# Performance work log

Hardware: AMD Instinct MI355X
Metric: run time of the kernel (lower is better)

## Reference

```python
import jax, jax.numpy as jnp
import numpy as np

K = 1024
D = 256
BETA = 0.25


def setup_inputs() -> dict:
    key = jax.random.key(0)
    k1, k2 = jax.random.split(key)
    latents = jax.random.normal(k1, (32, D, 32, 32), dtype=jnp.float32)
    # nn.Embedding init: uniform(-1/K, 1/K)
    embedding = jax.random.uniform(k2, (K, D), dtype=jnp.float32,
                                   minval=-1.0 / K, maxval=1.0 / K)
    return {"latents": latents, "embedding": embedding}


def reference(latents, embedding):
    # latents: [B, D, H, W] -> [B, H, W, D]
    x = jnp.transpose(latents, (0, 2, 3, 1))
    input_shape = x.shape
    flat = x.reshape(-1, D)  # [N, D]

    # squared-L2 distances to codebook: [N, K]
    distances = (jnp.sum(flat ** 2, axis=1, keepdims=True)
                 + jnp.sum(embedding ** 2, axis=1)
                 - 2.0 * flat @ embedding.T)
    encoding_indices = jnp.argmin(distances, axis=1)  # [N]

    # one-hot encodings (returned output); quantize via direct gather
    encodings = jax.nn.one_hot(encoding_indices, K, dtype=latents.dtype)  # [N, K]
    quantized = embedding[encoding_indices].reshape(input_shape)  # [B, H, W, D]

    e_latent_loss = jnp.mean((jax.lax.stop_gradient(quantized) - x) ** 2)
    q_latent_loss = jnp.mean((quantized - jax.lax.stop_gradient(x)) ** 2)
    loss = q_latent_loss + BETA * e_latent_loss

    # straight-through estimator
    quantized_st = x + jax.lax.stop_gradient(quantized - x)

    avg_probs = jnp.mean(encodings, axis=0)  # [K]
    perplexity = jnp.exp(-jnp.sum(avg_probs * jnp.log(avg_probs + 1e-10)))

    return (loss,
            jnp.transpose(quantized_st, (0, 3, 1, 2)),  # [B, D, H, W]
            perplexity,
            encodings)
```

## Files before the change

kernel.cpp:

```cpp
#include <hip/hip_runtime.h>
#include <stdint.h>
#include <math.h>

typedef float  f32x4 __attribute__((ext_vector_type(4)));
typedef float  f32x2 __attribute__((ext_vector_type(2)));
typedef short  s16x8 __attribute__((ext_vector_type(8)));
typedef short  s16x4 __attribute__((ext_vector_type(4)));

#define KC   1024
#define DD   256
#define NR   32768

#define WS_HIST   0
#define WS_ACC    4096
#define WS_E2     8192
#define WS_IDX    12288
#define WS_PANEL  143360
#define WS_PART   671744

#define ENC_OFF   8388610ULL

#define A_OFF   0
#define B_OFF   32768
#define E2_OFF  65536
#define SMEM_SZ 67584

#define GLD16(gp, lp) __builtin_amdgcn_global_load_lds(                      \
    (const __attribute__((address_space(1))) uint32_t*)(gp),                 \
    (__attribute__((address_space(3))) uint32_t*)(lp), 16, 0, 0)

#define WAITVM(N) asm volatile("s_waitcnt vmcnt(" #N ")" ::: "memory")
#define PHASEBAR() do { __builtin_amdgcn_s_barrier();                        \
                        __builtin_amdgcn_sched_barrier(0); } while (0)

__device__ __forceinline__ short f2bf(float f) {
    uint32_t u = __builtin_bit_cast(uint32_t, f);
    uint32_t r = (u + 0x7FFFu + ((u >> 16) & 1u)) >> 16;
    return (short)r;
}

__global__ void k_prep(const float* __restrict__ emb, char* __restrict__ ws) {
    int tid = threadIdx.x;
    if (blockIdx.x == 0) {
        uint32_t* hist = (uint32_t*)(ws + WS_HIST);
        #pragma unroll
        for (int j = 0; j < 4; j++) hist[tid * 4 + j] = 0u;
        if (tid < 2) ((float*)(ws + WS_ACC))[tid] = 0.f;
    }
    int wid = tid >> 6, lane = tid & 63;
    int code = blockIdx.x * 4 + wid;
    const float* row = emb + (size_t)code * DD;
    f32x4 v = *(const f32x4*)(row + lane * 4);
    s16x4 b;
    b[0] = f2bf(v.x); b[1] = f2bf(v.y); b[2] = f2bf(v.z); b[3] = f2bf(v.w);
    *(s16x4*)((short*)(ws + WS_PANEL) + (size_t)code * DD + lane * 4) = b;
    float ss = v.x * v.x + v.y * v.y + v.z * v.z + v.w * v.w;
    #pragma unroll
    for (int off = 1; off < 64; off <<= 1) ss += __shfl_xor(ss, off);
    if (lane == 0) ((float*)(ws + WS_E2))[code] = ss;
}

__global__ __launch_bounds__(256, 2) void k_argmin(const float* __restrict__ latents,
                                                   char* __restrict__ ws) {
    const char*  panelb = (const char*)(ws + WS_PANEL);
    const float* e2g    = (const float*)(ws + WS_E2);
    float*       acc    = (float*)(ws + WS_ACC);

    __shared__ __align__(16) char smem[SMEM_SZ];

    int t     = threadIdx.x;
    int lane  = t & 63;
    int wid   = t >> 6;
    int g     = lane >> 4, r16 = lane & 15;
    int rowgrp = blockIdx.x >> 1;
    int chalf  = blockIdx.x & 1;
    int nbase  = rowgrp * 128;
    int b      = nbase >> 10;
    int hwbase = nbase & 1023;
    const char* pbase = panelb + (size_t)chalf * 262144;

    if (t < 128) {
        f32x4 ev = *(const f32x4*)(e2g + chalf * 512 + t * 4);
        *(f32x4*)(smem + E2_OFF + t * 16) = ev;
    }

    float xs = 0.f;
    s16x8 af[2][8];
    int rg = (t & 15) * 4;
    int dp = (t >> 4) * 2;
    int wb = 4 * ((t >> 4) & 3);

    #pragma unroll
    for (int h = 0; h < 2; h++) {
        const float* base = latents + (size_t)b * 262144 + hwbase + h * 64 + rg;
        #pragma unroll
        for (int i = 0; i < 8; i++) {
            int d = dp + i * 32;
            f32x4 v0 = *(const f32x4*)(base + (size_t)d * 1024);
            f32x4 v1 = *(const f32x4*)(base + (size_t)(d + 1) * 1024);
            xs += v0.x*v0.x + v0.y*v0.y + v0.z*v0.z + v0.w*v0.w;
            xs += v1.x*v1.x + v1.y*v1.y + v1.z*v1.z + v1.w*v1.w;
            int qb = d >> 3;
            #pragma unroll
            for (int q = 0; q < 4; q++) {
                int slot = rg + q;
                uint32_t pk = (uint32_t)(uint16_t)f2bf(v0[q])
                            | ((uint32_t)(uint16_t)f2bf(v1[q]) << 16);
                int quad = qb ^ (slot & 7);
                *(uint32_t*)(smem + A_OFF + slot * 512 + quad * 16 + wb) = pk;
            }
        }
        __syncthreads();
        if ((wid >> 1) == h) {
            int slotbase = (wid & 1) * 32;
            #pragma unroll
            for (int rt = 0; rt < 2; rt++) {
                #pragma unroll
                for (int kt = 0; kt < 8; kt++) {
                    int slot = slotbase + rt * 16 + r16;
                    int quad = (kt * 4 + g) ^ (slot & 7);
                    af[rt][kt] = *(const s16x8*)(smem + A_OFF + slot * 512 + quad * 16);
                }
            }
        }
        __syncthreads();
    }
    if (chalf == 0) {
        #pragma unroll
        for (int off = 1; off < 64; off <<= 1) xs += __shfl_xor(xs, off);
        if (lane == 0) atomicAdd(acc + 0, xs);
    }

    float vmin[2][4];
    int   vidx[2][4];
    #pragma unroll
    for (int rt = 0; rt < 2; rt++)
        #pragma unroll
        for (int j = 0; j < 4; j++) { vmin[rt][j] = 3.4e38f; vidx[rt][j] = 0; }

    const float* E2l = (const float*)(smem + E2_OFF);
    int codeglob = chalf * 512;

    auto stage = [&](int c) {
        const char* srcc = pbase + (size_t)c * 8192;
        char* dstb = smem + B_OFF + (size_t)(c & 3) * 8192;
        #pragma unroll
        for (int i = 0; i < 2; i++) {
            uint32_t off = i * 4096 + wid * 1024;
            uint32_t so  = off + lane * 16;
            uint32_t ssw = so ^ (((so >> 9) & 7u) << 4);
            GLD16(srcc + ssw, dstb + off);
        }
    };
    auto compute = [&](int c) {
        int cbase = c * 16;
        float e2c = E2l[cbase + r16];
        const char* Bc = smem + B_OFF + (size_t)(c & 3) * 8192;
        s16x8 bf[8];
        #pragma unroll
        for (int kt = 0; kt < 8; kt++) {
            uint32_t byte = (uint32_t)(r16 * 512)
                          + (((uint32_t)(kt * 64 + g * 16)) ^ (((uint32_t)(r16 & 7)) << 4));
            bf[kt] = *(const s16x8*)(Bc + byte);
        }
        #pragma unroll
        for (int rt = 0; rt < 2; rt++) {
            f32x4 a4 = {0.f, 0.f, 0.f, 0.f};
            #pragma unroll
            for (int kt = 0; kt < 8; kt++)
                a4 = __builtin_amdgcn_mfma_f32_16x16x32_bf16(af[rt][kt], bf[kt], a4, 0, 0, 0);
            #pragma unroll
            for (int j = 0; j < 4; j++) {
                float s = e2c - 2.f * a4[j];
                bool better = s < vmin[rt][j];
                vmin[rt][j] = better ? s : vmin[rt][j];
                vidx[rt][j] = better ? (codeglob + cbase + r16) : vidx[rt][j];
            }
        }
    };

    stage(0); stage(1); stage(2);
    #pragma unroll 1
    for (int c = 0; c < 29; ++c) {
        WAITVM(4);
        PHASEBAR();
        compute(c);
        stage(c + 3);
    }
    WAITVM(4); PHASEBAR(); compute(29);
    WAITVM(2); PHASEBAR(); compute(30);
    WAITVM(0); PHASEBAR(); compute(31);

    uint2* part = (uint2*)(ws + WS_PART) + (size_t)chalf * NR;
    #pragma unroll
    for (int rt = 0; rt < 2; rt++) {
        #pragma unroll
        for (int j = 0; j < 4; j++) {
            float s = vmin[rt][j]; int ii = vidx[rt][j];
            #pragma unroll
            for (int off = 1; off < 16; off <<= 1) {
                float os = __shfl_xor(s, off);
                int   oi = __shfl_xor(ii, off);
                if (os < s || (os == s && oi < ii)) { s = os; ii = oi; }
            }
            if (r16 == 0) {
                int n = nbase + wid * 32 + rt * 16 + g * 4 + j;
                uint2 pv;
                pv.x = __builtin_bit_cast(uint32_t, s);
                pv.y = (uint32_t)ii;
                part[n] = pv;
            }
        }
    }
}

__global__ void k_comb(char* __restrict__ ws) {
    const uint2* part = (const uint2*)(ws + WS_PART);
    uint32_t* hist = (uint32_t*)(ws + WS_HIST);
    float*    acc  = (float*)(ws + WS_ACC);
    int*      idxo = (int*)(ws + WS_IDX);
    int n = blockIdx.x * 256 + threadIdx.x;
    uint2 p0 = part[n];
    uint2 p1 = part[NR + n];
    float s0 = __builtin_bit_cast(float, p0.x);
    float s1 = __builtin_bit_cast(float, p1.x);
    float s = (s1 < s0) ? s1 : s0;
    int  ii = (s1 < s0) ? (int)p1.y : (int)p0.y;
    idxo[n] = ii;
    atomicAdd(hist + ii, 1u);
    #pragma unroll
    for (int off = 1; off < 64; off <<= 1) s += __shfl_xor(s, off);
    if ((threadIdx.x & 63) == 0) atomicAdd(acc + 1, s);
}

__global__ void k_quant(const float* __restrict__ emb, const char* __restrict__ ws,
                        float* __restrict__ out) {
    const int* idx = (const int*)(ws + WS_IDX);
    int tid = threadIdx.x;
    int dg  = blockIdx.x & 63;
    int hwt = (blockIdx.x >> 6) & 3;
    int b   = blockIdx.x >> 8;
    int hw  = hwt * 256 + tid;
    int n   = b * 1024 + hw;
    int code = idx[n];
    f32x4 v = *(const f32x4*)(emb + (size_t)code * 256 + dg * 4);
    float* dst = out + 1 + (size_t)b * 262144 + (size_t)dg * 4096 + hw;
    dst[0] = v.x; dst[1024] = v.y; dst[2048] = v.z; dst[3072] = v.w;
}

__global__ void k_onehot(const char* __restrict__ ws, float* __restrict__ out) {
    const int* idx = (const int*)(ws + WS_IDX);
    __shared__ int lidx[8];
    int tid = threadIdx.x;
    int rbase = blockIdx.x * 8;
    if (tid < 8) lidx[tid] = idx[rbase + tid];
    __syncthreads();
    f32x2* enc = (f32x2*)(out + ENC_OFF);
    #pragma unroll
    for (int j = 0; j < 16; j++) {
        int linear = j * 256 + tid;
        int rl = linear >> 9, c2 = linear & 511;
        int id = lidx[rl];
        f32x2 v;
        v.x = (2 * c2     == id) ? 1.f : 0.f;
        v.y = (2 * c2 + 1 == id) ? 1.f : 0.f;
        enc[(size_t)(rbase + rl) * 512 + c2] = v;
    }
}

__global__ void k_final(const char* __restrict__ ws, float* __restrict__ out) {
    __shared__ float red[256];
    const uint32_t* hist = (const uint32_t*)(ws + WS_HIST);
    const float*    acc  = (const float*)(ws + WS_ACC);
    int tid = threadIdx.x;
    float part = 0.f;
    #pragma unroll
    for (int j = 0; j < 4; j++) {
        float p = (float)hist[tid * 4 + j] * (1.f / 32768.f);
        part += p * logf(p + 1e-10f);
    }
    red[tid] = part;
    __syncthreads();
    for (int s = 128; s > 0; s >>= 1) {
        if (tid < s) red[tid] += red[tid + s];
        __syncthreads();
    }
    if (tid == 0) {
        out[8388609] = expf(-red[0]);
        out[0] = 1.25f * (acc[0] + acc[1]) * (1.f / 8388608.f);
    }
}

extern "C" void kernel_launch(void* const* d_in, const int* in_sizes, int n_in,
                              void* d_out, int out_size, void* d_ws, size_t ws_size,
                              hipStream_t stream) {
    const float* latents = (const float*)d_in[0];
    const float* emb     = (const float*)d_in[1];
    float* out = (float*)d_out;
    char*  ws  = (char*)d_ws;

    hipLaunchKernelGGL(k_prep,   dim3(256),  dim3(256), 0, stream, emb, ws);
    hipLaunchKernelGGL(k_argmin, dim3(512),  dim3(256), 0, stream, latents, ws);
    hipLaunchKernelGGL(k_comb,   dim3(128),  dim3(256), 0, stream, ws);
    hipLaunchKernelGGL(k_quant,  dim3(8192), dim3(256), 0, stream, emb, ws, out);
    hipLaunchKernelGGL(k_onehot, dim3(4096), dim3(256), 0, stream, ws, out);
    hipLaunchKernelGGL(k_final,  dim3(1),    dim3(256), 0, stream, ws, out);
}
```

Measured before the change: 94.28 us.

## Stagger codebook chunk order per block, remap grid, and reswizzle LDS A tile

```diff
diff --git a/kernel.cpp b/kernel.cpp
--- a/kernel.cpp
+++ b/kernel.cpp
@@ -51,13 +51,16 @@
     int code = blockIdx.x * 4 + wid;
     const float* row = emb + (size_t)code * DD;
     f32x4 v = *(const f32x4*)(row + lane * 4);
-    s16x4 b;
-    b[0] = f2bf(v.x); b[1] = f2bf(v.y); b[2] = f2bf(v.z); b[3] = f2bf(v.w);
-    *(s16x4*)((short*)(ws + WS_PANEL) + (size_t)code * DD + lane * 4) = b;
+    uint32_t lo = (uint32_t)(uint16_t)f2bf(v.x) | ((uint32_t)(uint16_t)f2bf(v.y) << 16);
+    uint32_t hi = (uint32_t)(uint16_t)f2bf(v.z) | ((uint32_t)(uint16_t)f2bf(v.w) << 16);
+    uint32_t* dst = (uint32_t*)((short*)(ws + WS_PANEL) + (size_t)code * DD + lane * 4);
+    __builtin_nontemporal_store(lo, dst);
+    __builtin_nontemporal_store(hi, dst + 1);
     float ss = v.x * v.x + v.y * v.y + v.z * v.z + v.w * v.w;
     #pragma unroll
     for (int off = 1; off < 64; off <<= 1) ss += __shfl_xor(ss, off);
-    if (lane == 0) ((float*)(ws + WS_E2))[code] = ss;
+    if (lane == 0)
+        __builtin_nontemporal_store(ss, (float*)(ws + WS_E2) + code);
 }
 
 __global__ __launch_bounds__(256, 2) void k_argmin(const float* __restrict__ latents,
@@ -68,15 +71,16 @@
 
     __shared__ __align__(16) char smem[SMEM_SZ];
 
-    int t     = threadIdx.x;
-    int lane  = t & 63;
-    int wid   = t >> 6;
-    int g     = lane >> 4, r16 = lane & 15;
-    int rowgrp = blockIdx.x >> 1;
-    int chalf  = blockIdx.x & 1;
+    int t      = threadIdx.x;
+    int lane   = t & 63;
+    int wid    = t >> 6;
+    int g      = lane >> 4, r16 = lane & 15;
+    int rowgrp = blockIdx.x & 255;
+    int chalf  = blockIdx.x >> 8;
     int nbase  = rowgrp * 128;
     int b      = nbase >> 10;
     int hwbase = nbase & 1023;
+    int phase  = rowgrp & 31;
     const char* pbase = panelb + (size_t)chalf * 262144;
 
     if (t < 128) {
@@ -88,7 +92,6 @@
     s16x8 af[2][8];
     int rg = (t & 15) * 4;
     int dp = (t >> 4) * 2;
-    int wb = 4 * ((t >> 4) & 3);
 
     #pragma unroll
     for (int h = 0; h < 2; h++) {
@@ -106,8 +109,8 @@
                 int slot = rg + q;
                 uint32_t pk = (uint32_t)(uint16_t)f2bf(v0[q])
                             | ((uint32_t)(uint16_t)f2bf(v1[q]) << 16);
-                int quad = qb ^ (slot & 7);
-                *(uint32_t*)(smem + A_OFF + slot * 512 + quad * 16 + wb) = pk;
+                int quad = qb ^ (slot & 7) ^ ((slot >> 3) & 7);
+                *(uint32_t*)(smem + A_OFF + slot * 512 + quad * 16 + (d & 6) * 2) = pk;
             }
         }
         __syncthreads();
@@ -118,7 +121,7 @@
                 #pragma unroll
                 for (int kt = 0; kt < 8; kt++) {
                     int slot = slotbase + rt * 16 + r16;
-                    int quad = (kt * 4 + g) ^ (slot & 7);
+                    int quad = (kt * 4 + g) ^ (slot & 7) ^ ((slot >> 3) & 7);
                     af[rt][kt] = *(const s16x8*)(smem + A_OFF + slot * 512 + quad * 16);
                 }
             }
@@ -179,17 +182,17 @@
         }
     };
 
-    stage(0); stage(1); stage(2);
+    stage(phase); stage((phase + 1) & 31); stage((phase + 2) & 31);
     #pragma unroll 1
     for (int c = 0; c < 29; ++c) {
         WAITVM(4);
         PHASEBAR();
-        compute(c);
-        stage(c + 3);
-    }
-    WAITVM(4); PHASEBAR(); compute(29);
-    WAITVM(2); PHASEBAR(); compute(30);
-    WAITVM(0); PHASEBAR(); compute(31);
+        compute((c + phase) & 31);
+        stage((c + 3 + phase) & 31);
+    }
+    WAITVM(4); PHASEBAR(); compute((29 + phase) & 31);
+    WAITVM(2); PHASEBAR(); compute((30 + phase) & 31);
+    WAITVM(0); PHASEBAR(); compute((31 + phase) & 31);
 
     uint2* part = (uint2*)(ws + WS_PART) + (size_t)chalf * NR;
     #pragma unroll
```

Result: faster. 89.55 us, median of 2 (-5.0%).
